# Kernel tuning notes

Measured on AMD Instinct MI355X. Metric: run time of the kernel, lower is better.

Reference implementation:

```python
import jax, jax.numpy as jnp
import numpy as np

H = 1024   # hidden_size
S = 32768  # seq_len


def setup_inputs() -> dict:
    key = jax.random.key(0)
    k1, k2, k3, k4 = jax.random.split(key, 4)
    scale = 1.0 / np.sqrt(H)
    return {
        "hidden": jax.random.normal(k1, (H,), dtype=jnp.float32),
        "encoder_outputs": jax.random.normal(k2, (S, H), dtype=jnp.float32),
        "W": jax.random.normal(k3, (H, H), dtype=jnp.float32) * scale,
        "b": jax.random.normal(k4, (H,), dtype=jnp.float32) * scale,
    }


def reference(hidden, encoder_outputs, W, b):
    # method == 'general': energy_i = W @ enc_i + b ; score_i = hidden . energy_i
    # Vectorized: scores = (enc @ W^T + b) @ hidden  -> [S]
    energies = jnp.einsum("sh,dh->sd", encoder_outputs, W) + b  # [S, H]
    scores = energies @ hidden                                   # [S]
    attn = jax.nn.softmax(scores)                                 # softmax over seq_len
    return attn[None, None, :]                                    # [1, 1, S]
```

## Files before the change

kernel.cpp:

```cpp
#include <hip/hip_runtime.h>
#include <math.h>

#define H 1024
#define S 32768
#define NPART 16

#define WS_PART   0
#define WS_SCORES 16384
#define WS_PM     (16384 + S)
#define WS_PS     (16384 + S + 1024)

__global__ __launch_bounds__(256) void matvec_partial(const float* __restrict__ W,
                                                      const float* __restrict__ hidden,
                                                      float* __restrict__ ws) {
    float* part = ws + WS_PART;
    const int h  = blockIdx.x * 256 + threadIdx.x;
    const int by = blockIdx.y;
    const int d0 = by * 64;
    float acc = 0.f;
#pragma unroll 8
    for (int i = 0; i < 64; ++i) {
        const int d = d0 + i;
        acc += W[(size_t)d * H + h] * hidden[d];
    }
    part[by * H + h] = acc;
}

__global__ __launch_bounds__(256) void scores_partial(const float* __restrict__ enc,
                                                      float* __restrict__ ws) {
    float* part   = ws + WS_PART;
    float* scores = ws + WS_SCORES;
    float* pm     = ws + WS_PM;
    float* ps     = ws + WS_PS;

    const int tid  = threadIdx.x;
    const int lane = tid & 63;
    const int wv   = tid >> 6;
    const int blk  = blockIdx.x;

    __shared__ float vsh[H];
    {
        const float4* p4 = (const float4*)part;
        float4 a = make_float4(0.f, 0.f, 0.f, 0.f);
#pragma unroll
        for (int p = 0; p < NPART; ++p) {
            const float4 w = p4[p * (H / 4) + tid];
            a.x += w.x; a.y += w.y; a.z += w.z; a.w += w.w;
        }
        ((float4*)vsh)[tid] = a;
    }
    __syncthreads();

    const float4* v4 = (const float4*)vsh;
    float4 vf[4];
#pragma unroll
    for (int k = 0; k < 4; ++k) vf[k] = v4[lane + 64 * k];

    const int gw = blk * 4 + wv;
    float mw = -INFINITY, sw = 0.f;
#pragma unroll
    for (int it = 0; it < 8; ++it) {
        const int row = gw * 8 + it;
        const float4* e4 = (const float4*)(enc + (size_t)row * H);
        float a = 0.f;
#pragma unroll
        for (int k = 0; k < 4; ++k) {
            const float4 e = e4[lane + 64 * k];
            a += e.x * vf[k].x + e.y * vf[k].y + e.z * vf[k].z + e.w * vf[k].w;
        }
#pragma unroll
        for (int off = 32; off > 0; off >>= 1)
            a += __shfl_xor(a, off, 64);
        if (lane == 0) scores[row] = a;
        const float nm = fmaxf(mw, a);
        sw = sw * __expf(mw - nm) + __expf(a - nm);
        mw = nm;
    }

    __shared__ float sm[4], ss[4];
    if (lane == 0) { sm[wv] = mw; ss[wv] = sw; }
    __syncthreads();
    if (tid == 0) {
        float m = sm[0], s = ss[0];
#pragma unroll
        for (int i = 1; i < 4; ++i) {
            const float nm = fmaxf(m, sm[i]);
            s = s * __expf(m - nm) + ss[i] * __expf(sm[i] - nm);
            m = nm;
        }
        pm[blk] = m; ps[blk] = s;
    }
}

__global__ __launch_bounds__(256) void finalize(const float* __restrict__ ws,
                                                float* __restrict__ out) {
    const float* scores = ws + WS_SCORES;
    const float* pm     = ws + WS_PM;
    const float* ps     = ws + WS_PS;

    const int tid  = threadIdx.x;
    const int lane = tid & 63;
    const int wv   = tid >> 6;

    float m = -INFINITY, s = 0.f;
#pragma unroll
    for (int i = 0; i < 4; ++i) {
        const int idx = tid + i * 256;
        const float om = pm[idx], os = ps[idx];
        const float nm = fmaxf(m, om);
        s = s * __expf(m - nm) + os * __expf(om - nm);
        m = nm;
    }
#pragma unroll
    for (int off = 32; off > 0; off >>= 1) {
        const float om = __shfl_xor(m, off, 64);
        const float os = __shfl_xor(s, off, 64);
        const float nm = fmaxf(m, om);
        s = s * __expf(m - nm) + os * __expf(om - nm);
        m = nm;
    }
    __shared__ float sm[4], ss[4];
    if (lane == 0) { sm[wv] = m; ss[wv] = s; }
    __syncthreads();
    float M = sm[0], Ssum = ss[0];
#pragma unroll
    for (int i = 1; i < 4; ++i) {
        const float nm = fmaxf(M, sm[i]);
        Ssum = Ssum * __expf(M - nm) + ss[i] * __expf(sm[i] - nm);
        M = nm;
    }
    const float rs = 1.0f / Ssum;

    const int i = blockIdx.x * 256 + tid;
    out[i] = __expf(scores[i] - M) * rs;
}

extern "C" void kernel_launch(void* const* d_in, const int* in_sizes, int n_in,
                              void* d_out, int out_size, void* d_ws, size_t ws_size,
                              hipStream_t stream) {
    const float* hidden = (const float*)d_in[0];
    const float* enc    = (const float*)d_in[1];
    const float* W      = (const float*)d_in[2];
    float* out = (float*)d_out;
    float* ws  = (float*)d_ws;

    matvec_partial<<<dim3(H / 256, NPART), 256, 0, stream>>>(W, hidden, ws);
    scores_partial<<<1024, 256, 0, stream>>>(enc, ws);
    finalize<<<S / 256, 256, 0, stream>>>(ws, out);
}
```

Baseline: 208.3 us.

## Parallelize matvec more, hoist partial reduction to separate kernel, batch row loads

The W^T·hidden matvec now runs on 256 blocks instead of 64, each splitting its 64-row d-chunk across four waves and combining them in shared memory. The 16-way partial sum that every scores block used to redo is moved into a tiny reduce_v kernel, so the scores kernel reads the finished vector directly. The scores kernel also issues all eight rows' loads before the shuffle reductions, and replaces the online softmax with a max-then-sum. This adds one extra kernel launch and one more dependency in the chain in exchange for more load parallelism.

Result: faster. 203.5 us (-2.3%).

```diff
diff --git a/kernel.cpp b/kernel.cpp
--- a/kernel.cpp
+++ b/kernel.cpp
@@ -9,73 +9,96 @@
 #define WS_SCORES 16384
 #define WS_PM     (16384 + S)
 #define WS_PS     (16384 + S + 1024)
+#define WS_V      (16384 + S + 2048)
 
 __global__ __launch_bounds__(256) void matvec_partial(const float* __restrict__ W,
                                                       const float* __restrict__ hidden,
                                                       float* __restrict__ ws) {
     float* part = ws + WS_PART;
-    const int h  = blockIdx.x * 256 + threadIdx.x;
-    const int by = blockIdx.y;
-    const int d0 = by * 64;
+    const int t  = threadIdx.x;
+    const int l  = t & 63;
+    const int dg = t >> 6;
+    const int h  = blockIdx.x * 64 + l;
+    const int d0 = blockIdx.y * 64 + dg * 16;
+
     float acc = 0.f;
-#pragma unroll 8
-    for (int i = 0; i < 64; ++i) {
+#pragma unroll
+    for (int i = 0; i < 16; ++i) {
         const int d = d0 + i;
         acc += W[(size_t)d * H + h] * hidden[d];
     }
-    part[by * H + h] = acc;
+
+    __shared__ float red[4][64];
+    red[dg][l] = acc;
+    __syncthreads();
+    if (t < 64) {
+        part[blockIdx.y * H + blockIdx.x * 64 + l] =
+            red[0][l] + red[1][l] + red[2][l] + red[3][l];
+    }
+}
+
+__global__ __launch_bounds__(64) void reduce_v(float* __restrict__ ws) {
+    const float* part = ws + WS_PART;
+    float* v = ws + WS_V;
+    const int i = blockIdx.x * 64 + threadIdx.x;
+    const float4* p4 = (const float4*)part;
+    float4 a = p4[i];
+#pragma unroll
+    for (int p = 1; p < NPART; ++p) {
+        const float4 w = p4[p * (H / 4) + i];
+        a.x += w.x; a.y += w.y; a.z += w.z; a.w += w.w;
+    }
+    ((float4*)v)[i] = a;
 }
 
 __global__ __launch_bounds__(256) void scores_partial(const float* __restrict__ enc,
                                                       float* __restrict__ ws) {
-    float* part   = ws + WS_PART;
     float* scores = ws + WS_SCORES;
     float* pm     = ws + WS_PM;
     float* ps     = ws + WS_PS;
+    const float* v = ws + WS_V;
 
     const int tid  = threadIdx.x;
     const int lane = tid & 63;
     const int wv   = tid >> 6;
     const int blk  = blockIdx.x;
+    const int gw   = blk * 4 + wv;
+    const size_t row0 = (size_t)gw * 8;
 
-    __shared__ float vsh[H];
-    {
-        const float4* p4 = (const float4*)part;
-        float4 a = make_float4(0.f, 0.f, 0.f, 0.f);
-#pragma unroll
-        for (int p = 0; p < NPART; ++p) {
-            const float4 w = p4[p * (H / 4) + tid];
-            a.x += w.x; a.y += w.y; a.z += w.z; a.w += w.w;
-        }
-        ((float4*)vsh)[tid] = a;
-    }
-    __syncthreads();
-
-    const float4* v4 = (const float4*)vsh;
+    const float4* v4 = (const float4*)v;
     float4 vf[4];
 #pragma unroll
     for (int k = 0; k < 4; ++k) vf[k] = v4[lane + 64 * k];
 
-    const int gw = blk * 4 + wv;
-    float mw = -INFINITY, sw = 0.f;
+    float a[8];
 #pragma unroll
     for (int it = 0; it < 8; ++it) {
-        const int row = gw * 8 + it;
-        const float4* e4 = (const float4*)(enc + (size_t)row * H);
-        float a = 0.f;
+        const float4* e4 = (const float4*)(enc + (row0 + it) * H);
+        const float4 e0 = e4[lane];
+        const float4 e1 = e4[lane + 64];
+        const float4 e2 = e4[lane + 128];
+        const float4 e3 = e4[lane + 192];
+        float s0 = e0.x * vf[0].x + e0.y * vf[0].y + e0.z * vf[0].z + e0.w * vf[0].w;
+        float s1 = e1.x * vf[1].x + e1.y * vf[1].y + e1.z * vf[1].z + e1.w * vf[1].w;
+        float s2 = e2.x * vf[2].x + e2.y * vf[2].y + e2.z * vf[2].z + e2.w * vf[2].w;
+        float s3 = e3.x * vf[3].x + e3.y * vf[3].y + e3.z * vf[3].z + e3.w * vf[3].w;
+        a[it] = (s0 + s1) + (s2 + s3);
+    }
+
 #pragma unroll
-        for (int k = 0; k < 4; ++k) {
-            const float4 e = e4[lane + 64 * k];
-            a += e.x * vf[k].x + e.y * vf[k].y + e.z * vf[k].z + e.w * vf[k].w;
-        }
+    for (int it = 0; it < 8; ++it) {
 #pragma unroll
         for (int off = 32; off > 0; off >>= 1)
-            a += __shfl_xor(a, off, 64);
-        if (lane == 0) scores[row] = a;
-        const float nm = fmaxf(mw, a);
-        sw = sw * __expf(mw - nm) + __expf(a - nm);
-        mw = nm;
+            a[it] += __shfl_xor(a[it], off, 64);
+        if (lane == 0) scores[row0 + it] = a[it];
     }
+
+    float m01 = fmaxf(a[0], a[1]), m23 = fmaxf(a[2], a[3]);
+    float m45 = fmaxf(a[4], a[5]), m67 = fmaxf(a[6], a[7]);
+    const float mw = fmaxf(fmaxf(m01, m23), fmaxf(m45, m67));
+    float sw = 0.f;
+#pragma unroll
+    for (int it = 0; it < 8; ++it) sw += __expf(a[it] - mw);
 
     __shared__ float sm[4], ss[4];
     if (lane == 0) { sm[wv] = mw; ss[wv] = sw; }
@@ -144,7 +167,8 @@
     float* out = (float*)d_out;
     float* ws  = (float*)d_ws;
 
-    matvec_partial<<<dim3(H / 256, NPART), 256, 0, stream>>>(W, hidden, ws);
+    matvec_partial<<<dim3(16, 16), 256, 0, stream>>>(W, hidden, ws);
+    reduce_v<<<4, 64, 0, stream>>>(ws);
     scores_partial<<<1024, 256, 0, stream>>>(enc, ws);
     finalize<<<S / 256, 256, 0, stream>>>(ws, out);
 }
```
